# Performance work log

Measured on AMD Instinct MI355X. Metric: run time of the kernel, lower is better.

The kernel has to match this reference:

```python
import jax, jax.numpy as jnp
import numpy as np

W, H, C = 4096, 4096, 3


def setup_inputs() -> dict:
    key = jax.random.key(0)
    k_img, k_perm = jax.random.split(key)
    image = jax.random.normal(k_img, (W, H, C), dtype=jnp.float32)
    # Per-pixel random permutation of channels: argsort of iid uniforms along C
    # reproduces np.random.permutation(c) at every (i, j) deterministically.
    noise = jax.random.uniform(k_perm, (W, H, C))
    perm = jnp.argsort(noise, axis=-1).astype(jnp.int32)  # [W, H, C]
    return {"image": image, "perm": perm}


def reference(image, perm):
    # out[i, j, k] = image[i, j, perm[i, j, k]]  (per-pixel channel gather)
    return jnp.take_along_axis(image, perm, axis=-1)
```

## Files before the change

kernel.cpp:

```cpp
#include <hip/hip_runtime.h>


typedef float f32x4 __attribute__((ext_vector_type(4)));
typedef int   i32x4 __attribute__((ext_vector_type(4)));

__device__ __forceinline__ float sel8(float c0, float c1, float c2, float c3,
                                      float c4, float c5, float c6, float c7,
                                      int idx) {
    float s01 = (idx & 1) ? c1 : c0;
    float s23 = (idx & 1) ? c3 : c2;
    float s45 = (idx & 1) ? c5 : c4;
    float s67 = (idx & 1) ? c7 : c6;
    float s03 = (idx & 2) ? s23 : s01;
    float s47 = (idx & 2) ? s67 : s45;
    return (idx & 4) ? s47 : s03;
}

__global__ __launch_bounds__(256) void PerPixelChannelPermutation_kernel(
    const float* __restrict__ img, const i32x4* __restrict__ perm4,
    f32x4* __restrict__ out4, int nchunks, int n_elems) {
    const int c = blockIdx.x * blockDim.x + threadIdx.x;
    if (c >= nchunks) return;
    const int c4 = c * 4;

    const f32x4* img4 = (const f32x4*)img;
    const f32x4 v = img4[c];
    const i32x4 q = perm4[c];

    float pm2 = __shfl_up(v.z, 1);
    float pm1 = __shfl_up(v.w, 1);
    float nx0 = __shfl_down(v.x, 1);
    float nx1 = __shfl_down(v.y, 1);

    const int lane = threadIdx.x & 63;
    if (lane == 0) {
        int b = c4 - 2; if (b < 0) b = 0;
        pm2 = img[b];
        pm1 = img[b + 1];
    }
    if (lane == 63) {
        int b = c4 + 4; if (b > n_elems - 2) b = n_elems - 2;
        nx0 = img[b];
        nx1 = img[b + 1];
    }

    f32x4 o;
    {
        const unsigned n = (unsigned)(c4 + 0);
        const int idx = (int)((n / 3u) * 3u) - c4 + 2 + q.x;
        o.x = sel8(pm2, pm1, v.x, v.y, v.z, v.w, nx0, nx1, idx);
    }
    {
        const unsigned n = (unsigned)(c4 + 1);
        const int idx = (int)((n / 3u) * 3u) - c4 + 2 + q.y;
        o.y = sel8(pm2, pm1, v.x, v.y, v.z, v.w, nx0, nx1, idx);
    }
    {
        const unsigned n = (unsigned)(c4 + 2);
        const int idx = (int)((n / 3u) * 3u) - c4 + 2 + q.z;
        o.z = sel8(pm2, pm1, v.x, v.y, v.z, v.w, nx0, nx1, idx);
    }
    {
        const unsigned n = (unsigned)(c4 + 3);
        const int idx = (int)((n / 3u) * 3u) - c4 + 2 + q.w;
        o.w = sel8(pm2, pm1, v.x, v.y, v.z, v.w, nx0, nx1, idx);
    }

    out4[c] = o;
}

extern "C" void kernel_launch(void* const* d_in, const int* in_sizes, int n_in,
                              void* d_out, int out_size, void* d_ws, size_t ws_size,
                              hipStream_t stream) {
    const float* img   = (const float*)d_in[0];
    const i32x4* perm4 = (const i32x4*)d_in[1];
    f32x4*       out4  = (f32x4*)d_out;

    const int n_elems = in_sizes[0];
    const int nchunks = n_elems / 4;

    const int block = 256;
    const int grid  = (nchunks + block - 1) / block;
    PerPixelChannelPermutation_kernel<<<grid, block, 0, stream>>>(
        img, perm4, out4, nchunks, n_elems);
}
```

Measured before the change: 430.5 us.

## Process three chunks per thread with direct halo loads and nontemporal stores

Each thread now handles three float4 chunks strided by the block size, issuing all loads up front to raise memory-level parallelism. Cross-lane shuffles are replaced with direct float2 halo loads from neighbouring elements, which rely on the cache. The per-element division by 3 is replaced with a phase computed incrementally from c0 % 3. Output writes use nontemporal stores to avoid polluting the cache. In exchange the grid is smaller, register pressure is higher, and the unaligned float2 halo loads add redundant traffic.

```diff
diff --git a/kernel.cpp b/kernel.cpp
--- a/kernel.cpp
+++ b/kernel.cpp
@@ -1,8 +1,11 @@
 #include <hip/hip_runtime.h>
 
 
+typedef float f32x2 __attribute__((ext_vector_type(2)));
 typedef float f32x4 __attribute__((ext_vector_type(4)));
 typedef int   i32x4 __attribute__((ext_vector_type(4)));
+
+#define ITERS 3
 
 __device__ __forceinline__ float sel8(float c0, float c1, float c2, float c3,
                                       float c4, float c5, float c6, float c7,
@@ -19,54 +22,56 @@
 __global__ __launch_bounds__(256) void PerPixelChannelPermutation_kernel(
     const float* __restrict__ img, const i32x4* __restrict__ perm4,
     f32x4* __restrict__ out4, int nchunks, int n_elems) {
-    const int c = blockIdx.x * blockDim.x + threadIdx.x;
-    if (c >= nchunks) return;
-    const int c4 = c * 4;
+    const int tid = threadIdx.x;
+    const int c0  = blockIdx.x * (256 * ITERS) + tid;
+    if (c0 >= nchunks) return;
 
     const f32x4* img4 = (const f32x4*)img;
-    const f32x4 v = img4[c];
-    const i32x4 q = perm4[c];
 
-    float pm2 = __shfl_up(v.z, 1);
-    float pm1 = __shfl_up(v.w, 1);
-    float nx0 = __shfl_down(v.x, 1);
-    float nx1 = __shfl_down(v.y, 1);
+    f32x4 v[ITERS];
+    f32x2 lo[ITERS];
+    f32x2 hi[ITERS];
+    i32x4 q[ITERS];
 
-    const int lane = threadIdx.x & 63;
-    if (lane == 0) {
-        int b = c4 - 2; if (b < 0) b = 0;
-        pm2 = img[b];
-        pm1 = img[b + 1];
-    }
-    if (lane == 63) {
-        int b = c4 + 4; if (b > n_elems - 2) b = n_elems - 2;
-        nx0 = img[b];
-        nx1 = img[b + 1];
+#pragma unroll
+    for (int i = 0; i < ITERS; ++i) {
+        int c = c0 + i * 256;
+        if (c >= nchunks) c = c0;
+        const int c4 = c * 4;
+        v[i] = img4[c];
+        int bl = c4 - 2; if (bl < 0) bl = 0;
+        int bh = c4 + 4; if (bh > n_elems - 2) bh = n_elems - 2;
+        lo[i] = *(const f32x2*)(img + bl);
+        hi[i] = *(const f32x2*)(img + bh);
+        q[i]  = perm4[c];
     }
 
-    f32x4 o;
-    {
-        const unsigned n = (unsigned)(c4 + 0);
-        const int idx = (int)((n / 3u) * 3u) - c4 + 2 + q.x;
-        o.x = sel8(pm2, pm1, v.x, v.y, v.z, v.w, nx0, nx1, idx);
+    const int p0 = c0 % 3;
+#pragma unroll
+    for (int i = 0; i < ITERS; ++i) {
+        const int c = c0 + i * 256;
+        int p = p0 + i;
+        if (p >= 3) p -= 3;
+
+        const int off0 = 2 - p;
+        const int off3 = 5 - p;
+        const int off1 = (p == 0) ? 2 : ((p == 1) ? 1 : 3);
+        const int off2 = (p == 0) ? 2 : ((p == 1) ? 4 : 3);
+
+        f32x4 o;
+        o.x = sel8(lo[i].x, lo[i].y, v[i].x, v[i].y, v[i].z, v[i].w,
+                   hi[i].x, hi[i].y, off0 + q[i].x);
+        o.y = sel8(lo[i].x, lo[i].y, v[i].x, v[i].y, v[i].z, v[i].w,
+                   hi[i].x, hi[i].y, off1 + q[i].y);
+        o.z = sel8(lo[i].x, lo[i].y, v[i].x, v[i].y, v[i].z, v[i].w,
+                   hi[i].x, hi[i].y, off2 + q[i].z);
+        o.w = sel8(lo[i].x, lo[i].y, v[i].x, v[i].y, v[i].z, v[i].w,
+                   hi[i].x, hi[i].y, off3 + q[i].w);
+
+        if (c < nchunks) {
+            __builtin_nontemporal_store(o, &out4[c]);
+        }
     }
-    {
-        const unsigned n = (unsigned)(c4 + 1);
-        const int idx = (int)((n / 3u) * 3u) - c4 + 2 + q.y;
-        o.y = sel8(pm2, pm1, v.x, v.y, v.z, v.w, nx0, nx1, idx);
-    }
-    {
-        const unsigned n = (unsigned)(c4 + 2);
-        const int idx = (int)((n / 3u) * 3u) - c4 + 2 + q.z;
-        o.z = sel8(pm2, pm1, v.x, v.y, v.z, v.w, nx0, nx1, idx);
-    }
-    {
-        const unsigned n = (unsigned)(c4 + 3);
-        const int idx = (int)((n / 3u) * 3u) - c4 + 2 + q.w;
-        o.w = sel8(pm2, pm1, v.x, v.y, v.z, v.w, nx0, nx1, idx);
-    }
-
-    out4[c] = o;
 }
 
 extern "C" void kernel_launch(void* const* d_in, const int* in_sizes, int n_in,
@@ -80,7 +85,8 @@
     const int nchunks = n_elems / 4;
 
     const int block = 256;
-    const int grid  = (nchunks + block - 1) / block;
+    const int per_block = block * ITERS;
+    const int grid = (nchunks + per_block - 1) / per_block;
     PerPixelChannelPermutation_kernel<<<grid, block, 0, stream>>>(
         img, perm4, out4, nchunks, n_elems);
 }
```

New measurement: 449.4 us. 1.04x slower.
